# Kernel optimization log

Hardware: AMD Instinct MI355X
Metric: run time of the kernel (lower is better)

Reference implementation:

```python
import jax, jax.numpy as jnp
import numpy as np

ALPHA = 50.0
BETA = 0.5
EPS = 1e-6

def setup_inputs() -> dict:
    key = jax.random.key(0)
    k1, k2, k3 = jax.random.split(key, 3)
    N, D = 131072, 512
    output1 = jax.random.normal(k1, (N, D), dtype=jnp.float32)
    output2 = jax.random.normal(k2, (N, D), dtype=jnp.float32)
    target = jax.random.randint(k3, (N,), 0, 2, dtype=jnp.int64)
    return {"output1": output1, "output2": output2, "target": target}

def reference(output1, output2, target):
    # per-pair cosine similarity (torch.nn.CosineSimilarity, dim=1, eps=1e-6)
    dot = jnp.sum(output1 * output2, axis=1)
    denom = jnp.maximum(jnp.linalg.norm(output1, axis=1) * jnp.linalg.norm(output2, axis=1), EPS)
    d = dot / denom  # [N]
    # binomial deviance terms
    pos = (2.0 / BETA) * jax.nn.softplus(-BETA * (d - 0.5))
    neg = (2.0 / ALPHA) * jax.nn.softplus(ALPHA * (d - 2.0))
    is_pos = (target == 1)
    num_pos = jnp.sum(is_pos)
    num_neg = target.shape[0] - num_pos
    pos_loss = jnp.sum(jnp.where(is_pos, pos, 0.0)) / jnp.maximum(num_pos, 1)
    neg_loss = jnp.sum(jnp.where(is_pos, 0.0, neg)) / jnp.maximum(num_neg, 1)
    return pos_loss + neg_loss
```

## Files before the change

kernel.cpp:

```cpp
#include <hip/hip_runtime.h>
#include <math.h>

#define N_ROWS 131072
#define D 512
#define BLOCKS 512
#define WPB 4
#define NWAVES (BLOCKS * WPB)
#define ROWS_PER_WAVE (N_ROWS / NWAVES)
#define N_IT (ROWS_PER_WAVE / 2)
#define EPS 1e-6f

#define WAIT_VM(N) __builtin_amdgcn_s_waitcnt(0x0F70 | ((N) & 0xF) | ((((N) >> 4) & 3) << 14))

#define GLD16(gp, lp) __builtin_amdgcn_global_load_lds(                         \
    (const __attribute__((address_space(1))) unsigned int*)(gp),                \
    (__attribute__((address_space(3))) unsigned int*)(lp), 16, 0, 0)

__device__ __forceinline__ float softplusf(float x) {
    if (x > 0.0f) return x + log1pf(__expf(-x));
    return log1pf(__expf(x));
}

__device__ __forceinline__ void stage4k(const float* __restrict__ g, float* l, int lane) {
    #pragma unroll
    for (int c = 0; c < 4; ++c)
        GLD16(g + c * 256 + lane * 4, l + c * 256 + lane * 4);
}

__global__ __launch_bounds__(256) void binloss_main(
    const float* __restrict__ o1, const float* __restrict__ o2,
    const int* __restrict__ target,
    float* __restrict__ sums, int* __restrict__ icnt,
    unsigned int* __restrict__ done, float* __restrict__ out) {

    __shared__ __align__(16) float lds[WPB][2][2][1024];
    __shared__ float sPos[WPB], sNeg[WPB];
    __shared__ int sCnt[WPB];

    const int lane = threadIdx.x & 63;
    const int wave = threadIdx.x >> 6;
    const int gwave = blockIdx.x * WPB + wave;
    const int rowBase = gwave * ROWS_PER_WAVE;
    const int sub = lane & 31;
    const int rl = lane >> 5;

    const int myT = target[rowBase + lane];

    stage4k(o1 + (size_t)rowBase * D, &lds[wave][0][0][0], lane);
    stage4k(o2 + (size_t)rowBase * D, &lds[wave][0][1][0], lane);

    float posAcc = 0.0f, negAcc = 0.0f;
    int posCnt = 0;

    for (int k = 0; k < N_IT; ++k) {
        const int b = k & 1;
        if (k + 1 < N_IT) {
            const size_t nr = (size_t)(rowBase + 2 * (k + 1)) * D;
            stage4k(o1 + nr, &lds[wave][1 - b][0][0], lane);
            stage4k(o2 + nr, &lds[wave][1 - b][1][0], lane);
            WAIT_VM(8);
        } else {
            WAIT_VM(0);
        }

        const float* A = &lds[wave][b][0][rl * 512];
        const float* B = &lds[wave][b][1][rl * 512];
        float dot = 0.0f, s1 = 0.0f, s2 = 0.0f;
        #pragma unroll
        for (int j = 0; j < 4; ++j) {
            float4 a = *(const float4*)(A + sub * 4 + j * 128);
            float4 v = *(const float4*)(B + sub * 4 + j * 128);
            dot += a.x * v.x + a.y * v.y + a.z * v.z + a.w * v.w;
            s1  += a.x * a.x + a.y * a.y + a.z * a.z + a.w * a.w;
            s2  += v.x * v.x + v.y * v.y + v.z * v.z + v.w * v.w;
        }

        #pragma unroll
        for (int off = 16; off > 0; off >>= 1) {
            dot += __shfl_xor(dot, off);
            s1  += __shfl_xor(s1, off);
            s2  += __shfl_xor(s2, off);
        }

        const int t0 = __shfl(myT, 2 * k);
        const int t1 = __shfl(myT, 2 * k + 1);
        if (sub == 0) {
            float d = dot / fmaxf(sqrtf(s1) * sqrtf(s2), EPS);
            int t = rl ? t1 : t0;
            if (t == 1) { posAcc += 4.0f * softplusf(-0.5f * (d - 0.5f)); posCnt++; }
            else        { negAcc += 0.04f * softplusf(50.0f * (d - 2.0f)); }
        }
    }

    #pragma unroll
    for (int off = 32; off > 0; off >>= 1) {
        posAcc += __shfl_xor(posAcc, off);
        negAcc += __shfl_xor(negAcc, off);
        posCnt += __shfl_xor(posCnt, off);
    }

    if (lane == 0) { sPos[wave] = posAcc; sNeg[wave] = negAcc; sCnt[wave] = posCnt; }
    __syncthreads();
    if (threadIdx.x == 0) {
        float p = sPos[0] + sPos[1] + sPos[2] + sPos[3];
        float n = sNeg[0] + sNeg[1] + sNeg[2] + sNeg[3];
        int c = sCnt[0] + sCnt[1] + sCnt[2] + sCnt[3];
        atomicAdd(&sums[0], p);
        atomicAdd(&sums[1], n);
        atomicAdd(&icnt[0], c);
        __threadfence();
        unsigned int old = atomicAdd(done, 1u);
        if (old == (unsigned int)(gridDim.x - 1)) {
            __threadfence();
            float ps = __hip_atomic_load(&sums[0], __ATOMIC_RELAXED, __HIP_MEMORY_SCOPE_AGENT);
            float ns = __hip_atomic_load(&sums[1], __ATOMIC_RELAXED, __HIP_MEMORY_SCOPE_AGENT);
            int np = __hip_atomic_load(&icnt[0], __ATOMIC_RELAXED, __HIP_MEMORY_SCOPE_AGENT);
            int nn = N_ROWS - np;
            out[0] = ps / (float)(np > 1 ? np : 1) + ns / (float)(nn > 1 ? nn : 1);
        }
    }
}

extern "C" void kernel_launch(void* const* d_in, const int* in_sizes, int n_in,
                              void* d_out, int out_size, void* d_ws, size_t ws_size,
                              hipStream_t stream) {
    const float* o1 = (const float*)d_in[0];
    const float* o2 = (const float*)d_in[1];
    const int* tgt = (const int*)d_in[2];
    float* out = (float*)d_out;
    float* sums = (float*)d_ws;
    int* cnt = (int*)((char*)d_ws + 8);
    unsigned int* done = (unsigned int*)((char*)d_ws + 12);

    hipMemsetAsync(d_ws, 0, 16, stream);
    binloss_main<<<BLOCKS, 256, 0, stream>>>(o1, o2, tgt, sums, cnt, done, out);
}
```

Baseline: 537.5 us.

## Replace LDS-staged loads with register double-buffered global loads and more blocks

Drops the global_load_lds staging through shared memory and instead loads float4 fragments straight into registers, ping-ponging between two register buffers so the next row pair's loads overlap the current compute. The grid grows from 512 to 2048 blocks with a launch-bounds occupancy hint, giving 16 rows per wave instead of 64. Softplus becomes branchless. This removes the LDS round-trip and explicit waitcnt management but leans on the compiler to schedule the register prefetch, and it adds more atomics in the final reduction.

```diff
diff --git a/kernel.cpp b/kernel.cpp
--- a/kernel.cpp
+++ b/kernel.cpp
@@ -3,37 +3,65 @@
 
 #define N_ROWS 131072
 #define D 512
-#define BLOCKS 512
+#define BLOCKS 2048
 #define WPB 4
 #define NWAVES (BLOCKS * WPB)
 #define ROWS_PER_WAVE (N_ROWS / NWAVES)
 #define N_IT (ROWS_PER_WAVE / 2)
 #define EPS 1e-6f
 
-#define WAIT_VM(N) __builtin_amdgcn_s_waitcnt(0x0F70 | ((N) & 0xF) | ((((N) >> 4) & 3) << 14))
-
-#define GLD16(gp, lp) __builtin_amdgcn_global_load_lds(                         \
-    (const __attribute__((address_space(1))) unsigned int*)(gp),                \
-    (__attribute__((address_space(3))) unsigned int*)(lp), 16, 0, 0)
-
 __device__ __forceinline__ float softplusf(float x) {
-    if (x > 0.0f) return x + log1pf(__expf(-x));
-    return log1pf(__expf(x));
+    return fmaxf(x, 0.0f) + log1pf(__expf(-fabsf(x)));
 }
 
-__device__ __forceinline__ void stage4k(const float* __restrict__ g, float* l, int lane) {
+struct Frag {
+    float4 a[4];
+    float4 b[4];
+};
+
+__device__ __forceinline__ void issue_loads(const float* __restrict__ o1,
+                                            const float* __restrict__ o2,
+                                            size_t elem, Frag& f) {
+    const float* p1 = o1 + elem;
+    const float* p2 = o2 + elem;
     #pragma unroll
-    for (int c = 0; c < 4; ++c)
-        GLD16(g + c * 256 + lane * 4, l + c * 256 + lane * 4);
+    for (int j = 0; j < 4; ++j) {
+        f.a[j] = *(const float4*)(p1 + j * 128);
+        f.b[j] = *(const float4*)(p2 + j * 128);
+    }
 }
 
-__global__ __launch_bounds__(256) void binloss_main(
+__device__ __forceinline__ void process(const Frag& f, int t0, int t1, int rl, int sub,
+                                        float& posAcc, float& negAcc, int& posCnt) {
+    float dot = 0.0f, s1 = 0.0f, s2 = 0.0f;
+    #pragma unroll
+    for (int j = 0; j < 4; ++j) {
+        float4 a = f.a[j];
+        float4 v = f.b[j];
+        dot += a.x * v.x + a.y * v.y + a.z * v.z + a.w * v.w;
+        s1  += a.x * a.x + a.y * a.y + a.z * a.z + a.w * a.w;
+        s2  += v.x * v.x + v.y * v.y + v.z * v.z + v.w * v.w;
+    }
+    #pragma unroll
+    for (int off = 16; off > 0; off >>= 1) {
+        dot += __shfl_xor(dot, off);
+        s1  += __shfl_xor(s1, off);
+        s2  += __shfl_xor(s2, off);
+    }
+    if (sub == 0) {
+        float d = dot / fmaxf(sqrtf(s1) * sqrtf(s2), EPS);
+        int t = rl ? t1 : t0;
+        if (t == 1) { posAcc += 4.0f * softplusf(-0.5f * (d - 0.5f)); posCnt++; }
+        else        { negAcc += 0.04f * softplusf(50.0f * (d - 2.0f)); }
+    }
+}
+
+__global__ __launch_bounds__(256, 4) void binloss_main(
     const float* __restrict__ o1, const float* __restrict__ o2,
     const int* __restrict__ target,
     float* __restrict__ sums, int* __restrict__ icnt,
     unsigned int* __restrict__ done, float* __restrict__ out) {
 
-    __shared__ __align__(16) float lds[WPB][2][2][1024];
     __shared__ float sPos[WPB], sNeg[WPB];
     __shared__ int sCnt[WPB];
 
@@ -44,60 +72,32 @@
     const int sub = lane & 31;
     const int rl = lane >> 5;
 
-    const int myT = target[rowBase + lane];
+    const int myT = target[rowBase + (lane & (ROWS_PER_WAVE - 1))];
 
-    stage4k(o1 + (size_t)rowBase * D, &lds[wave][0][0][0], lane);
-    stage4k(o2 + (size_t)rowBase * D, &lds[wave][0][1][0], lane);
+    const size_t colOff = (size_t)sub * 4;
 
     float posAcc = 0.0f, negAcc = 0.0f;
     int posCnt = 0;
 
-    for (int k = 0; k < N_IT; ++k) {
-        const int b = k & 1;
-        if (k + 1 < N_IT) {
-            const size_t nr = (size_t)(rowBase + 2 * (k + 1)) * D;
-            stage4k(o1 + nr, &lds[wave][1 - b][0][0], lane);
-            stage4k(o2 + nr, &lds[wave][1 - b][1][0], lane);
-            WAIT_VM(8);
-        } else {
-            WAIT_VM(0);
-        }
+    Frag fA, fB;
+    issue_loads(o1, o2, (size_t)(rowBase + rl) * D + colOff, fA);
 
-        const float* A = &lds[wave][b][0][rl * 512];
-        const float* B = &lds[wave][b][1][rl * 512];
-        float dot = 0.0f, s1 = 0.0f, s2 = 0.0f;
-        #pragma unroll
-        for (int j = 0; j < 4; ++j) {
-            float4 a = *(const float4*)(A + sub * 4 + j * 128);
-            float4 v = *(const float4*)(B + sub * 4 + j * 128);
-            dot += a.x * v.x + a.y * v.y + a.z * v.z + a.w * v.w;
-            s1  += a.x * a.x + a.y * a.y + a.z * a.z + a.w * a.w;
-            s2  += v.x * v.x + v.y * v.y + v.z * v.z + v.w * v.w;
-        }
+    for (int k = 0; k < N_IT; k += 2) {
+        issue_loads(o1, o2, (size_t)(rowBase + 2 * (k + 1) + rl) * D + colOff, fB);
 
-        #pragma unroll
-        for (int off = 16; off > 0; off >>= 1) {
-            dot += __shfl_xor(dot, off);
-            s1  += __shfl_xor(s1, off);
-            s2  += __shfl_xor(s2, off);
-        }
+        process(fA, __shfl(myT, 2 * k), __shfl(myT, 2 * k + 1), rl, sub,
+                posAcc, negAcc, posCnt);
 
-        const int t0 = __shfl(myT, 2 * k);
-        const int t1 = __shfl(myT, 2 * k + 1);
-        if (sub == 0) {
-            float d = dot / fmaxf(sqrtf(s1) * sqrtf(s2), EPS);
-            int t = rl ? t1 : t0;
-            if (t == 1) { posAcc += 4.0f * softplusf(-0.5f * (d - 0.5f)); posCnt++; }
-            else        { negAcc += 0.04f * softplusf(50.0f * (d - 2.0f)); }
-        }
+        if (k + 2 < N_IT)
+            issue_loads(o1, o2, (size_t)(rowBase + 2 * (k + 2) + rl) * D + colOff, fA);
+
+        process(fB, __shfl(myT, 2 * k + 2), __shfl(myT, 2 * k + 3), rl, sub,
+                posAcc, negAcc, posCnt);
     }
 
-    #pragma unroll
-    for (int off = 32; off > 0; off >>= 1) {
-        posAcc += __shfl_xor(posAcc, off);
-        negAcc += __shfl_xor(negAcc, off);
-        posCnt += __shfl_xor(posCnt, off);
-    }
+    posAcc += __shfl_xor(posAcc, 32);
+    negAcc += __shfl_xor(negAcc, 32);
+    posCnt += __shfl_xor(posCnt, 32);
 
     if (lane == 0) { sPos[wave] = posAcc; sNeg[wave] = negAcc; sCnt[wave] = posCnt; }
     __syncthreads();
```

Result: slower. 588.9 us (+9.6%).
